# Performance work log

Hardware: AMD Instinct MI355X
Metric: run time of the kernel (lower is better)

Reference implementation:

```python
import jax, jax.numpy as jnp
import numpy as np

DILATION = 1  # module init dilation


def _pd_indexing1d(x, d, dilation):
    # x: (B, C, T) float; d: (B, 1, T) float pitch-dependent dilation factors
    B, C, T = x.shape
    dil = jnp.clip((d * dilation).astype(jnp.int32), 1)          # (B,1,T), min 1
    idx = jnp.arange(T, dtype=jnp.int32)[None, None, :]          # (1,1,T)
    idxP = jnp.abs(idx - dil) % T                                # past indices
    idxF0 = idx + dil
    # torch sets overflowed idx to -(idx % T) - 1, i.e. wraps to T - 1 - (idx % T)
    idxF = jnp.where(idxF0 >= T, T - 1 - (idxF0 % T), idxF0)     # future indices
    xP = jnp.take_along_axis(x, jnp.broadcast_to(idxP, x.shape), axis=2)
    xF = jnp.take_along_axis(x, jnp.broadcast_to(idxF, x.shape), axis=2)
    return xP, x, xF


def setup_inputs() -> dict:
    key = jax.random.key(0)
    k1, k2, k3, k4, k5, k6 = jax.random.split(key, 6)
    B, Cin, Cout, T = 8, 512, 512, 8192
    x = jax.random.normal(k1, (B, Cin, T), dtype=jnp.float32)
    d = jax.random.uniform(k2, (B, 1, T), dtype=jnp.float32)
    s = 1.0 / np.sqrt(Cin)
    W0 = jax.random.uniform(k3, (Cout, Cin), jnp.float32, -s, s)  # conv with bias
    b0 = jax.random.uniform(k4, (Cout,), jnp.float32, -s, s)
    W1 = jax.random.uniform(k5, (Cout, Cin), jnp.float32, -s, s)  # no bias
    W2 = jax.random.uniform(k6, (Cout, Cin), jnp.float32, -s, s)  # no bias
    return {"x": x, "d": d, "W0": W0, "b0": b0, "W1": W1, "W2": W2}


def reference(x, d, W0, b0, W1, W2):
    xP, xC, xF = _pd_indexing1d(x, d, DILATION)
    # three 1x1 convs (channel-mixing matmuls), summed; bias only on first conv
    out = jnp.einsum('oc,bct->bot', W0, xP) + b0[None, :, None]
    out = out + jnp.einsum('oc,bct->bot', W1, xC)
    out = out + jnp.einsum('oc,bct->bot', W2, xF)
    return out
```

## Files before the change

### kernel.cpp

```cpp
#include <hip/hip_runtime.h>

#define TT 8192
#define CIN 512
#define COUT 512
#define NB 8
#define KTOT 1536
#define NT 24

typedef __attribute__((ext_vector_type(4))) float f32x4;
typedef __attribute__((ext_vector_type(8))) short bf16x8;
typedef __attribute__((ext_vector_type(8))) unsigned short u16x8;

#define GLD16(g, l) __builtin_amdgcn_global_load_lds(                      \
    (const __attribute__((address_space(1))) void*)(g),                    \
    (__attribute__((address_space(3))) void*)(l), 16, 0, 0)

#define CFENCE() asm volatile("" ::: "memory")
#define SBAR() do { CFENCE(); __builtin_amdgcn_s_barrier(); CFENCE(); } while (0)
#define VMCNT4() asm volatile("s_waitcnt vmcnt(4)" ::: "memory")
#define VMCNT0() asm volatile("s_waitcnt vmcnt(0)" ::: "memory")
#define MFMA(a_, b_, c_) __builtin_amdgcn_mfma_f32_16x16x32_bf16((a_), (b_), (c_), 0, 0, 0)

__device__ inline unsigned short f2bf(float f) {
  union { float f; unsigned int u; } v; v.f = f;
  unsigned int u = v.u;
  unsigned int r = (u + 0x7FFFu + ((u >> 16) & 1u)) >> 16;
  return (unsigned short)r;
}

__global__ void k_convert_w(const float* __restrict__ W0, const float* __restrict__ W1,
                            const float* __restrict__ W2, unsigned short* __restrict__ Wb) {
  int i = blockIdx.x * 256 + threadIdx.x;
  if (i >= COUT * CIN) return;
  const float* Ws = blockIdx.y == 0 ? W0 : (blockIdx.y == 1 ? W1 : W2);
  int o = i >> 9, c = i & 511;
  Wb[(size_t)o * KTOT + blockIdx.y * CIN + c] = f2bf(Ws[i]);
}

__global__ void k_transpose(const float* __restrict__ x, unsigned short* __restrict__ xbT,
                            int b_base) {
  int b = b_base + blockIdx.z;
  const float* xb = x + (size_t)b * CIN * TT;
  unsigned short* xo = xbT + (size_t)blockIdx.z * TT * CIN;
  __shared__ float tile[64][65];
  int t0 = blockIdx.x * 64, c0 = blockIdx.y * 64;
  int tid = threadIdx.x;
#pragma unroll
  for (int it = 0; it < 16; ++it) {
    int L = it * 256 + tid;
    int c = L >> 6, t = L & 63;
    tile[c][t] = xb[(size_t)(c0 + c) * TT + (t0 + t)];
  }
  __syncthreads();
#pragma unroll
  for (int it = 0; it < 16; ++it) {
    int L = it * 256 + tid;
    int t = L >> 6, c = L & 63;
    xo[(size_t)(t0 + t) * CIN + (c0 + c)] = f2bf(tile[c][t]);
  }
}

__global__ __launch_bounds__(512) void k_gemm256(
    const unsigned short* __restrict__ Wb, const unsigned short* __restrict__ xbT,
    const float* __restrict__ d, const float* __restrict__ bias,
    float* __restrict__ out) {
  __shared__ __align__(16) unsigned short As[2][256 * 64];
  __shared__ __align__(16) unsigned short Bs[2][256 * 64];
  const int b = blockIdx.z;
  const unsigned short* xb = xbT + (size_t)b * TT * CIN;
  const int t0 = blockIdx.x * 256;
  const int row0 = blockIdx.y * 256;
  const int tid = threadIdx.x;
  const int lane = tid & 63, wid = tid >> 6;
  const int wr = wid >> 2, wc = wid & 3;
  const int l15 = lane & 15, kg = lane >> 4;

  const int srow = tid >> 3;
  const int cSrc8 = (((tid & 7) ^ ((tid >> 4) & 7))) * 8;
  int aOff[4];
  int bOff[3][4];
#pragma unroll
  for (int j = 0; j < 4; ++j) {
    int r = j * 64 + srow;
    aOff[j] = (row0 + r) * KTOT + cSrc8;
    int t = t0 + r;
    float dv = d[(size_t)b * TT + t];
    int dil = (int)dv; if (dil < 1) dil = 1;
    int p = t - dil; if (p < 0) p = -p; p &= (TT - 1);
    int f0 = t + dil;
    int f = (f0 >= TT) ? (TT - 1 - (f0 & (TT - 1))) : f0;
    bOff[0][j] = p * CIN + cSrc8;
    bOff[1][j] = t * CIN + cSrc8;
    bOff[2][j] = f * CIN + cSrc8;
  }

  const int s7 = l15 >> 1;
  const int chunk0 = (kg ^ (s7 & 3)) + (s7 & 4);
  const int dK = (l15 & 8) ? -32 : 32;
  int aRd[2][4], bRd[2][2];
#pragma unroll
  for (int mh = 0; mh < 2; ++mh)
#pragma unroll
    for (int mi = 0; mi < 4; ++mi)
      aRd[mh][mi] = (wr * 128 + mh * 64 + mi * 16 + l15) * 64 + chunk0 * 8;
#pragma unroll
  for (int nh = 0; nh < 2; ++nh)
#pragma unroll
    for (int ni = 0; ni < 2; ++ni)
      bRd[nh][ni] = (wc * 64 + nh * 32 + ni * 16 + l15) * 64 + chunk0 * 8;

#define STAGE_A2(tc_, buf_, jp_) do {                                         \
    _Pragma("unroll") for (int j = 2 * (jp_); j < 2 * (jp_) + 2; ++j)         \
      GLD16(Wb + aOff[j] + (tc_) * 64, &As[buf_][j * 4096 + wid * 512]);      \
  } while (0)
#define STAGE_B2(tc_, buf_, jp_) do {                                         \
    _Pragma("unroll") for (int j = 2 * (jp_); j < 2 * (jp_) + 2; ++j)         \
      GLD16(xb + bOff[(tc_) >> 3][j] + ((tc_) & 7) * 64,                      \
            &Bs[buf_][j * 4096 + wid * 512]);                                 \
  } while (0)

  STAGE_A2(0, 0, 0); STAGE_A2(0, 0, 1);
  STAGE_B2(0, 0, 0); STAGE_B2(0, 0, 1);
  STAGE_B2(1, 1, 0); STAGE_B2(1, 1, 1);
  VMCNT4();
  SBAR();

  bf16x8 af0[4][2], af1[4][2], bfr[2][2];
  f32x4 acc[8][4] = {};

#pragma unroll 2
  for (int tc = 0; tc < NT; ++tc) {
    const int cur = tc & 1;
#pragma unroll
    for (int mi = 0; mi < 4; ++mi) {
      af0[mi][0] = *(const bf16x8*)&As[cur][aRd[0][mi]];
      af0[mi][1] = *(const bf16x8*)&As[cur][aRd[0][mi] + dK];
    }
#pragma unroll
    for (int ni = 0; ni < 2; ++ni) {
      bfr[ni][0] = *(const bf16x8*)&Bs[cur][bRd[0][ni]];
      bfr[ni][1] = *(const bf16x8*)&Bs[cur][bRd[0][ni] + dK];
    }
    if (tc + 1 < NT) STAGE_A2(tc + 1, cur ^ 1, 0);
    SBAR();
    __builtin_amdgcn_s_setprio(1);
#pragma unroll
    for (int mi = 0; mi < 4; ++mi)
#pragma unroll
      for (int ni = 0; ni < 2; ++ni) {
        acc[mi][ni] = MFMA(af0[mi][0], bfr[ni][0], acc[mi][ni]);
        acc[mi][ni] = MFMA(af0[mi][1], bfr[ni][1], acc[mi][ni]);
      }
    __builtin_amdgcn_s_setprio(0);
    SBAR();
#pragma unroll
    for (int mi = 0; mi < 4; ++mi) {
      af1[mi][0] = *(const bf16x8*)&As[cur][aRd[1][mi]];
      af1[mi][1] = *(const bf16x8*)&As[cur][aRd[1][mi] + dK];
    }
    if (tc + 1 < NT) STAGE_A2(tc + 1, cur ^ 1, 1);
    SBAR();
    __builtin_amdgcn_s_setprio(1);
#pragma unroll
    for (int mi = 0; mi < 4; ++mi)
#pragma unroll
      for (int ni = 0; ni < 2; ++ni) {
        acc[4 + mi][ni] = MFMA(af1[mi][0], bfr[ni][0], acc[4 + mi][ni]);
        acc[4 + mi][ni] = MFMA(af1[mi][1], bfr[ni][1], acc[4 + mi][ni]);
      }
    __builtin_amdgcn_s_setprio(0);
#pragma unroll
    for (int ni = 0; ni < 2; ++ni) {
      bfr[ni][0] = *(const bf16x8*)&Bs[cur][bRd[1][ni]];
      bfr[ni][1] = *(const bf16x8*)&Bs[cur][bRd[1][ni] + dK];
    }
    SBAR();
    __builtin_amdgcn_s_setprio(1);
#pragma unroll
    for (int mi = 0; mi < 4; ++mi)
#pragma unroll
      for (int ni = 0; ni < 2; ++ni) {
        acc[mi][2 + ni] = MFMA(af0[mi][0], bfr[ni][0], acc[mi][2 + ni]);
        acc[mi][2 + ni] = MFMA(af0[mi][1], bfr[ni][1], acc[mi][2 + ni]);
      }
    __builtin_amdgcn_s_setprio(0);
    if (tc + 2 < NT) { STAGE_B2(tc + 2, cur, 0); STAGE_B2(tc + 2, cur, 1); }
    __builtin_amdgcn_s_setprio(1);
#pragma unroll
    for (int mi = 0; mi < 4; ++mi)
#pragma unroll
      for (int ni = 0; ni < 2; ++ni) {
        acc[4 + mi][2 + ni] = MFMA(af1[mi][0], bfr[ni][0], acc[4 + mi][2 + ni]);
        acc[4 + mi][2 + ni] = MFMA(af1[mi][1], bfr[ni][1], acc[4 + mi][2 + ni]);
      }
    __builtin_amdgcn_s_setprio(0);
    if (tc + 2 < NT) { VMCNT4(); }
    else if (tc + 1 < NT) { VMCNT0(); }
    SBAR();
  }

  float* ob = out + (size_t)b * COUT * TT;
#pragma unroll
  for (int mh = 0; mh < 2; ++mh)
#pragma unroll
    for (int mi = 0; mi < 4; ++mi) {
      int m0 = row0 + wr * 128 + mh * 64 + mi * 16 + kg * 4;
#pragma unroll
      for (int nh = 0; nh < 2; ++nh)
#pragma unroll
        for (int ni = 0; ni < 2; ++ni) {
          int t = t0 + wc * 64 + nh * 32 + ni * 16 + l15;
          f32x4 v = acc[mh * 4 + mi][nh * 2 + ni];
#pragma unroll
          for (int j = 0; j < 4; ++j)
            ob[(size_t)(m0 + j) * TT + t] = v[j] + bias[m0 + j];
        }
    }
}

__global__ __launch_bounds__(256) void k_gemm(
    const unsigned short* __restrict__ Wb, const unsigned short* __restrict__ xbT,
    const float* __restrict__ d, const float* __restrict__ bias,
    float* __restrict__ out, int b_base) {
  __shared__ __align__(16) unsigned short As[128 * 32];
  __shared__ __align__(16) unsigned short Bs[128 * 32];
  int b = b_base + blockIdx.z;
  const unsigned short* xb = xbT + (size_t)blockIdx.z * TT * CIN;
  int row0 = blockIdx.x * 128;
  int t0 = blockIdx.y * 128;
  int tid = threadIdx.x;
  int lane = tid & 63, wid = tid >> 6;
  int wr = wid >> 1, wc = wid & 1;
  int l15 = lane & 15, kg = lane >> 4;
  int rs = tid >> 2, cch = tid & 3;

  const unsigned short* aw[2];
  const unsigned short* bw[2][3];
#pragma unroll
  for (int h = 0; h < 2; ++h) {
    int r = rs + h * 64;
    int cs = cch ^ ((r >> 1) & 3);
    aw[h] = Wb + (size_t)(row0 + r) * KTOT + cs * 8;
    int t = t0 + r;
    float dv = d[(size_t)b * TT + t];
    int dil = (int)dv; if (dil < 1) dil = 1;
    int p = t - dil; if (p < 0) p = -p; p &= (TT - 1);
    int f0 = t + dil;
    int f = (f0 >= TT) ? (TT - 1 - (f0 & (TT - 1))) : f0;
    bw[h][0] = xb + (size_t)p * CIN + cs * 8;
    bw[h][1] = xb + (size_t)t * CIN + cs * 8;
    bw[h][2] = xb + (size_t)f * CIN + cs * 8;
  }
  unsigned short* aDst[2];
  unsigned short* bDst[2];
#pragma unroll
  for (int h = 0; h < 2; ++h) {
    aDst[h] = As + h * 2048 + wid * 512;
    bDst[h] = Bs + h * 2048 + wid * 512;
  }
  int aoff[4], boff[4];
#pragma unroll
  for (int mi = 0; mi < 4; ++mi) {
    int r = wr * 64 + mi * 16 + l15;
    aoff[mi] = r * 32 + (kg ^ ((r >> 1) & 3)) * 8;
  }
#pragma unroll
  for (int ni = 0; ni < 4; ++ni) {
    int r = wc * 64 + ni * 16 + l15;
    boff[ni] = r * 32 + (kg ^ ((r >> 1) & 3)) * 8;
  }
  f32x4 acc[4][4] = {};
#pragma unroll
  for (int s = 0; s < 3; ++s) {
    for (int kt = 0; kt < 16; ++kt) {
      int koff = kt * 32;
#pragma unroll
      for (int h = 0; h < 2; ++h) {
        GLD16(aw[h] + s * CIN + koff, aDst[h]);
        GLD16(bw[h][s] + koff, bDst[h]);
      }
      __syncthreads();
      bf16x8 af[4], bf[4];
#pragma unroll
      for (int mi = 0; mi < 4; ++mi) af[mi] = *(const bf16x8*)(&As[aoff[mi]]);
#pragma unroll
      for (int ni = 0; ni < 4; ++ni) bf[ni] = *(const bf16x8*)(&Bs[boff[ni]]);
#pragma unroll
      for (int mi = 0; mi < 4; ++mi)
#pragma unroll
        for (int ni = 0; ni < 4; ++ni)
          acc[mi][ni] = MFMA(af[mi], bf[ni], acc[mi][ni]);
      __syncthreads();
    }
  }
  float* ob = out + (size_t)b * COUT * TT;
#pragma unroll
  for (int mi = 0; mi < 4; ++mi) {
    int m0 = row0 + wr * 64 + mi * 16 + kg * 4;
#pragma unroll
    for (int ni = 0; ni < 4; ++ni) {
      int t = t0 + wc * 64 + ni * 16 + l15;
#pragma unroll
      for (int j = 0; j < 4; ++j) {
        ob[(size_t)(m0 + j) * TT + t] = acc[mi][ni][j] + bias[m0 + j];
      }
    }
  }
}

extern "C" void kernel_launch(void* const* d_in, const int* in_sizes, int n_in,
                              void* d_out, int out_size, void* d_ws, size_t ws_size,
                              hipStream_t stream) {
  const float* x  = (const float*)d_in[0];
  const float* d  = (const float*)d_in[1];
  const float* W0 = (const float*)d_in[2];
  const float* b0 = (const float*)d_in[3];
  const float* W1 = (const float*)d_in[4];
  const float* W2 = (const float*)d_in[5];
  float* out = (float*)d_out;

  char* ws = (char*)d_ws;
  unsigned short* Wb  = (unsigned short*)ws;
  unsigned short* xbT = (unsigned short*)(ws + (2u << 20));
  const size_t SZ_XBT1 = (size_t)TT * CIN * 2;
  const size_t NEED_FULL = (size_t)(2u << 20) + (size_t)NB * SZ_XBT1;
  const size_t NEED_MIN  = (size_t)(2u << 20) + SZ_XBT1;

  if (ws_size >= NEED_MIN) {
    k_convert_w<<<dim3(1024, 3), 256, 0, stream>>>(W0, W1, W2, Wb);
    if (ws_size >= NEED_FULL) {
      k_transpose<<<dim3(TT / 64, CIN / 64, NB), 256, 0, stream>>>(x, xbT, 0);
      k_gemm256<<<dim3(TT / 256, COUT / 256, NB), 512, 0, stream>>>(Wb, xbT, d, b0, out);
    } else {
      for (int b = 0; b < NB; ++b) {
        k_transpose<<<dim3(TT / 64, CIN / 64, 1), 256, 0, stream>>>(x, xbT, b);
        k_gemm<<<dim3(COUT / 128, TT / 128, 1), 256, 0, stream>>>(Wb, xbT, d, b0, out, b);
      }
    }
  } else {
    for (int b = 0; b < NB; ++b) {
      k_transpose<<<dim3(TT / 64, CIN / 64, 1), 256, 0, stream>>>(x, xbT, b);
      k_gemm<<<dim3(COUT / 128, TT / 128, 1), 256, 0, stream>>>(Wb, xbT, d, b0, out, b);
    }
  }
}
```

Baseline: 144.5 us.

## Collapse GEMM main-loop phases to cut barriers per K-step

The main loop now loads all B fragments for both column halves up front. It issues both A prefetch halves together, waits on LDS with lgkmcnt(0), and takes a single barrier. After that it issues the B prefetch for step tc+2 and runs all MFMAs in two large blocks. This replaces the earlier four-phase interleave, which had several s_barriers per iteration. The goal is to reduce barrier stalls and keep MFMA issue denser. In exchange it holds more fragment registers live, which may raise VGPR pressure, and it loses some fine-grained overlap between LDS reads and MFMA work.

```diff
diff --git a/kernel.cpp b/kernel.cpp
--- a/kernel.cpp
+++ b/kernel.cpp
@@ -19,6 +19,7 @@
 #define SBAR() do { CFENCE(); __builtin_amdgcn_s_barrier(); CFENCE(); } while (0)
 #define VMCNT4() asm volatile("s_waitcnt vmcnt(4)" ::: "memory")
 #define VMCNT0() asm volatile("s_waitcnt vmcnt(0)" ::: "memory")
+#define LGKM0() asm volatile("s_waitcnt lgkmcnt(0)" ::: "memory")
 #define MFMA(a_, b_, c_) __builtin_amdgcn_mfma_f32_16x16x32_bf16((a_), (b_), (c_), 0, 0, 0)
 
 __device__ inline unsigned short f2bf(float f) {
@@ -125,73 +126,51 @@
   VMCNT4();
   SBAR();
 
-  bf16x8 af0[4][2], af1[4][2], bfr[2][2];
+  bf16x8 af0[4][2], af1[4][2], bf0[2][2], bf1[2][2];
   f32x4 acc[8][4] = {};
 
 #pragma unroll 2
   for (int tc = 0; tc < NT; ++tc) {
     const int cur = tc & 1;
 #pragma unroll
+    for (int ni = 0; ni < 2; ++ni) {
+      bf0[ni][0] = *(const bf16x8*)&Bs[cur][bRd[0][ni]];
+      bf0[ni][1] = *(const bf16x8*)&Bs[cur][bRd[0][ni] + dK];
+      bf1[ni][0] = *(const bf16x8*)&Bs[cur][bRd[1][ni]];
+      bf1[ni][1] = *(const bf16x8*)&Bs[cur][bRd[1][ni] + dK];
+    }
+    if (tc + 1 < NT) { STAGE_A2(tc + 1, cur ^ 1, 0); STAGE_A2(tc + 1, cur ^ 1, 1); }
+    LGKM0();
+    SBAR();
+    if (tc + 2 < NT) { STAGE_B2(tc + 2, cur, 0); STAGE_B2(tc + 2, cur, 1); }
+#pragma unroll
     for (int mi = 0; mi < 4; ++mi) {
       af0[mi][0] = *(const bf16x8*)&As[cur][aRd[0][mi]];
       af0[mi][1] = *(const bf16x8*)&As[cur][aRd[0][mi] + dK];
     }
 #pragma unroll
-    for (int ni = 0; ni < 2; ++ni) {
-      bfr[ni][0] = *(const bf16x8*)&Bs[cur][bRd[0][ni]];
-      bfr[ni][1] = *(const bf16x8*)&Bs[cur][bRd[0][ni] + dK];
-    }
-    if (tc + 1 < NT) STAGE_A2(tc + 1, cur ^ 1, 0);
-    SBAR();
-    __builtin_amdgcn_s_setprio(1);
-#pragma unroll
-    for (int mi = 0; mi < 4; ++mi)
-#pragma unroll
-      for (int ni = 0; ni < 2; ++ni) {
-        acc[mi][ni] = MFMA(af0[mi][0], bfr[ni][0], acc[mi][ni]);
-        acc[mi][ni] = MFMA(af0[mi][1], bfr[ni][1], acc[mi][ni]);
-      }
-    __builtin_amdgcn_s_setprio(0);
-    SBAR();
-#pragma unroll
     for (int mi = 0; mi < 4; ++mi) {
       af1[mi][0] = *(const bf16x8*)&As[cur][aRd[1][mi]];
       af1[mi][1] = *(const bf16x8*)&As[cur][aRd[1][mi] + dK];
     }
-    if (tc + 1 < NT) STAGE_A2(tc + 1, cur ^ 1, 1);
-    SBAR();
     __builtin_amdgcn_s_setprio(1);
 #pragma unroll
     for (int mi = 0; mi < 4; ++mi)
 #pragma unroll
       for (int ni = 0; ni < 2; ++ni) {
-        acc[4 + mi][ni] = MFMA(af1[mi][0], bfr[ni][0], acc[4 + mi][ni]);
-        acc[4 + mi][ni] = MFMA(af1[mi][1], bfr[ni][1], acc[4 + mi][ni]);
-      }
-    __builtin_amdgcn_s_setprio(0);
-#pragma unroll
-    for (int ni = 0; ni < 2; ++ni) {
-      bfr[ni][0] = *(const bf16x8*)&Bs[cur][bRd[1][ni]];
-      bfr[ni][1] = *(const bf16x8*)&Bs[cur][bRd[1][ni] + dK];
-    }
-    SBAR();
-    __builtin_amdgcn_s_setprio(1);
+        acc[mi][ni] = MFMA(af0[mi][0], bf0[ni][0], acc[mi][ni]);
+        acc[mi][ni] = MFMA(af0[mi][1], bf0[ni][1], acc[mi][ni]);
+        acc[mi][2 + ni] = MFMA(af0[mi][0], bf1[ni][0], acc[mi][2 + ni]);
+        acc[mi][2 + ni] = MFMA(af0[mi][1], bf1[ni][1], acc[mi][2 + ni]);
+      }
 #pragma unroll
     for (int mi = 0; mi < 4; ++mi)
 #pragma unroll
       for (int ni = 0; ni < 2; ++ni) {
-        acc[mi][2 + ni] = MFMA(af0[mi][0], bfr[ni][0], acc[mi][2 + ni]);
-        acc[mi][2 + ni] = MFMA(af0[mi][1], bfr[ni][1], acc[mi][2 + ni]);
-      }
-    __builtin_amdgcn_s_setprio(0);
-    if (tc + 2 < NT) { STAGE_B2(tc + 2, cur, 0); STAGE_B2(tc + 2, cur, 1); }
-    __builtin_amdgcn_s_setprio(1);
-#pragma unroll
-    for (int mi = 0; mi < 4; ++mi)
-#pragma unroll
-      for (int ni = 0; ni < 2; ++ni) {
-        acc[4 + mi][2 + ni] = MFMA(af1[mi][0], bfr[ni][0], acc[4 + mi][2 + ni]);
-        acc[4 + mi][2 + ni] = MFMA(af1[mi][1], bfr[ni][1], acc[4 + mi][2 + ni]);
+        acc[4 + mi][ni] = MFMA(af1[mi][0], bf0[ni][0], acc[4 + mi][ni]);
+        acc[4 + mi][ni] = MFMA(af1[mi][1], bf0[ni][1], acc[4 + mi][ni]);
+        acc[4 + mi][2 + ni] = MFMA(af1[mi][0], bf1[ni][0], acc[4 + mi][2 + ni]);
+        acc[4 + mi][2 + ni] = MFMA(af1[mi][1], bf1[ni][1], acc[4 + mi][2 + ni]);
       }
     __builtin_amdgcn_s_setprio(0);
     if (tc + 2 < NT) { VMCNT4(); }
```

Result: slower. 166.9 us (+15.5%).
